# Kernel optimization log

Measured on AMD Instinct MI355X. Metric: run time of the kernel, lower is better.

Reference implementation:

```python
import jax, jax.numpy as jnp
import numpy as np

TEMPERATURE = 1.0


def setup_inputs() -> dict:
    key = jax.random.key(0)
    kq, kk, kv = jax.random.split(key, 3)
    shape = (2, 16, 2048, 64)  # B, H, L, D
    q = jax.random.normal(kq, shape, dtype=jnp.float32)
    k = jax.random.normal(kk, shape, dtype=jnp.float32)
    v = jax.random.normal(kv, shape, dtype=jnp.float32)
    return {"q": q, "k": k, "v": v}


def reference(q, k, v):
    # q, k, v: [B, H, L, D]
    L = q.shape[2]
    # scores: [B, H, L, L]; note: divided by temperature, NOT sqrt(D), per source
    scores = jnp.einsum("bhqd,bhkd->bhqk", q, k) / TEMPERATURE
    # causal mask: position j > i masked with -inf
    causal = jnp.tril(jnp.ones((L, L), dtype=bool))  # True = keep
    scores = jnp.where(causal, scores, -jnp.inf)
    attn = jax.nn.softmax(scores, axis=-1)
    out = jnp.einsum("bhqk,bhkd->bhqd", attn, v)
    return out
```

## Files before the change

kernel.cpp:

```cpp
#include <hip/hip_runtime.h>
#include <math.h>


typedef __attribute__((ext_vector_type(8))) _Float16 f16x8;
typedef __attribute__((ext_vector_type(4))) _Float16 f16x4;
typedef __attribute__((ext_vector_type(4))) float f32x4;
typedef __attribute__((ext_vector_type(16))) float f32x16;
typedef unsigned short u16;
typedef unsigned int u32;
typedef __attribute__((ext_vector_type(8))) u16 u16x8;
typedef __attribute__((ext_vector_type(4))) u32 u32x4;

constexpr int Lq = 2048;
constexpr int Dd = 64;
constexpr int KT = 64;
constexpr int BH = 32;
constexpr float LOG2E = 1.44269504088896f;

#define SWZB(row, bcol) ((((row) * 128) + (bcol)) ^ (((row) & 7) << 4))
#define SWZB64(row, bcol) ((((row) * 64) + (bcol)) ^ ((((row) >> 1) & 3) << 4))

#define GLOAD_LDS16(g, l)                                                     \
  __builtin_amdgcn_global_load_lds(                                           \
      (const __attribute__((address_space(1))) void*)(g),                     \
      (__attribute__((address_space(3))) void*)(l), 16, 0, 0)

static __device__ __forceinline__ u16 f2h(float x) {
  return __builtin_bit_cast(u16, (_Float16)x);
}

static __device__ __forceinline__ float tmax16(const f32x16& v) {
  float a = fmaxf(v[0], v[1]), b = fmaxf(v[2], v[3]);
  float c = fmaxf(v[4], v[5]), d = fmaxf(v[6], v[7]);
  float e = fmaxf(v[8], v[9]), f = fmaxf(v[10], v[11]);
  float g = fmaxf(v[12], v[13]), h = fmaxf(v[14], v[15]);
  a = fmaxf(a, b); c = fmaxf(c, d); e = fmaxf(e, f); g = fmaxf(g, h);
  return fmaxf(fmaxf(a, c), fmaxf(e, g));
}
static __device__ __forceinline__ float tsum16(const f32x16& v) {
  float a = v[0] + v[1], b = v[2] + v[3], c = v[4] + v[5], d = v[6] + v[7];
  float e = v[8] + v[9], f = v[10] + v[11], g = v[12] + v[13], h = v[14] + v[15];
  a += b; c += d; e += f; g += h;
  return (a + c) + (e + g);
}

constexpr int PREP_KB = (BH * Lq * Dd) / (256 * 16);

__global__ __launch_bounds__(256)
void attn_prep(const float* __restrict__ K, const float* __restrict__ V,
               u16* __restrict__ Kh, u16* __restrict__ VTh) {
  const int b = blockIdx.x;
  const int tid = threadIdx.x;
  if (b < PREP_KB) {
    const size_t base = ((size_t)b * 256 + tid) * 16;
    const f32x4* src = reinterpret_cast<const f32x4*>(K + base);
    u16x8 o0, o1;
    #pragma unroll
    for (int i = 0; i < 2; ++i) {
      const f32x4 a = src[i];
      #pragma unroll
      for (int j = 0; j < 4; ++j) o0[i * 4 + j] = f2h(a[j]);
    }
    #pragma unroll
    for (int i = 0; i < 2; ++i) {
      const f32x4 a = src[2 + i];
      #pragma unroll
      for (int j = 0; j < 4; ++j) o1[i * 4 + j] = f2h(a[j]);
    }
    *reinterpret_cast<u16x8*>(Kh + base) = o0;
    *reinterpret_cast<u16x8*>(Kh + base + 8) = o1;
  } else {
    __shared__ u16 lt[64][66];
    const int vb = b - PREP_KB;
    const int h = vb >> 5, tt = vb & 31;
    const float* Vt = V + ((size_t)h * Lq + tt * 64) * Dd;
    const int r = tid & 63, dg = tid >> 6;
    #pragma unroll
    for (int i = 0; i < 4; ++i) {
      const f32x4 a = *reinterpret_cast<const f32x4*>(Vt + (size_t)r * Dd + dg * 16 + i * 4);
      #pragma unroll
      for (int j = 0; j < 2; ++j) {
        const unsigned two =
            (unsigned)f2h(a[2 * j]) | ((unsigned)f2h(a[2 * j + 1]) << 16);
        *reinterpret_cast<unsigned*>(&lt[r][dg * 16 + i * 4 + j * 2]) = two;
      }
    }
    __syncthreads();
    const int d = tid >> 2, kq = tid & 3;
    u16x8 w0, w1;
    #pragma unroll
    for (int j = 0; j < 8; ++j) w0[j] = lt[kq * 16 + j][d];
    #pragma unroll
    for (int j = 0; j < 8; ++j) w1[j] = lt[kq * 16 + 8 + j][d];
    u16* dst = VTh + ((size_t)h * Dd + d) * Lq + tt * 64 + kq * 16;
    *reinterpret_cast<u16x8*>(dst) = w0;
    *reinterpret_cast<u16x8*>(dst + 8) = w1;
  }
}

__global__ __launch_bounds__(64)
void attn_main(const float* __restrict__ Q, float* __restrict__ O,
               const u16* __restrict__ Kh, const u16* __restrict__ VTh) {
  __shared__ char ksA[2][4096];
  __shared__ char vtA[2][4096];
  __shared__ float bc[32];

  const int lane = threadIdx.x;
  const int l31  = lane & 31;
  const int hi   = lane >> 5;

  const int b = blockIdx.x;
  const int chunk = 63 - (b >> 5);
  const int h = b & 31;

  const float* Qb = Q + (size_t)h * Lq * Dd;
  float*       Ob = O + (size_t)h * Lq * Dd;
  const u16*   Kb = Kh + (size_t)h * Lq * Dd;
  const u16*   Vb = VTh + (size_t)h * Dd * Lq;

  const int T    = chunk + 1;
  const int qrow = chunk * 32;

  f16x8 qf[4];
  #pragma unroll
  for (int kc = 0; kc < 4; ++kc) {
    const float* qp = Qb + (size_t)(qrow + l31) * Dd + kc * 16 + hi * 8;
    const f32x4 a = *reinterpret_cast<const f32x4*>(qp);
    const f32x4 c = *reinterpret_cast<const f32x4*>(qp + 4);
    f16x8 q8;
    #pragma unroll
    for (int e = 0; e < 4; ++e) {
      q8[e]     = (_Float16)(a[e] * LOG2E);
      q8[e + 4] = (_Float16)(c[e] * LOG2E);
    }
    qf[kc] = q8;
  }

  float m = -INFINITY, lsum = 0.f;
  f32x16 o0, o1;
  #pragma unroll
  for (int e = 0; e < 16; ++e) { o0[e] = 0.f; o1[e] = 0.f; }

  const int rrK = lane >> 3;
  const int c0K = (lane & 7) ^ (rrK & 7);
  const int rrV = lane >> 2;
  const int c0V = (lane & 3) ^ ((lane >> 3) & 3);

#define STAGE(t_, buf_)                                                       \
  do {                                                                        \
    const u16* Kt_ = Kb + (size_t)(t_) * 32 * Dd;                             \
    _Pragma("unroll")                                                         \
    for (int it = 0; it < 4; ++it) {                                          \
      GLOAD_LDS16(Kt_ + (size_t)(it * 8 + rrK) * Dd + c0K * 8,                \
                  &ksA[buf_][it * 1024 + lane * 16]);                         \
    }                                                                         \
    _Pragma("unroll")                                                         \
    for (int it = 0; it < 4; ++it) {                                          \
      GLOAD_LDS16(Vb + (size_t)(it * 16 + rrV) * Lq + (t_) * 32 + c0V * 8,    \
                  &vtA[buf_][it * 1024 + lane * 16]);                         \
    }                                                                         \
  } while (0)

  STAGE(0, 0);

  int cur = 0;
  #pragma unroll 1
  for (int t = 0; t < T; ++t) {
    const bool pf = (t + 1 < T);
    if (pf) {
      STAGE(t + 1, cur ^ 1);
      asm volatile("s_waitcnt vmcnt(8)" ::: "memory");
    } else {
      asm volatile("s_waitcnt vmcnt(0)" ::: "memory");
    }
    __builtin_amdgcn_sched_barrier(0);
    const char* kb = ksA[cur];
    const char* vb = vtA[cur];
    const bool last = (t == T - 1);

    f32x16 st0;
    #pragma unroll
    for (int e = 0; e < 16; ++e) st0[e] = 0.f;
    __builtin_amdgcn_s_setprio(1);
    #pragma unroll
    for (int kc = 0; kc < 4; ++kc) {
      const f16x8 kf = *reinterpret_cast<const f16x8*>(
          kb + SWZB(l31, kc * 32 + hi * 16));
      st0 = __builtin_amdgcn_mfma_f32_32x32x16_f16(kf, qf[kc], st0, 0, 0, 0);
    }
    __builtin_amdgcn_s_setprio(0);

    if (last) {
      #pragma unroll
      for (int r = 0; r < 16; ++r) {
        const int crow = (r & 3) + 8 * (r >> 2) + 4 * hi;
        if (crow > l31) st0[r] = -INFINITY;
      }
    }

    float pm = tmax16(st0);
    pm = fmaxf(pm, __shfl_xor(pm, 32));

    if (__any(pm > m + 8.f * LOG2E)) {
      const float mn = fmaxf(m, pm);
      const float sc = exp2f(m - mn);
      m = mn;
      lsum *= sc;
      if (hi == 0) bc[l31] = sc;
      const f32x4 s0 = *reinterpret_cast<const f32x4*>(&bc[4 * hi]);
      const f32x4 s1 = *reinterpret_cast<const f32x4*>(&bc[8 + 4 * hi]);
      const f32x4 s2 = *reinterpret_cast<const f32x4*>(&bc[16 + 4 * hi]);
      const f32x4 s3 = *reinterpret_cast<const f32x4*>(&bc[24 + 4 * hi]);
      #pragma unroll
      for (int r = 0; r < 16; ++r) {
        const float fac = (r < 4) ? s0[r & 3] : (r < 8) ? s1[r & 3]
                        : (r < 12) ? s2[r & 3] : s3[r & 3];
        o0[r] *= fac;
        o1[r] *= fac;
      }
    }

    #pragma unroll
    for (int r = 0; r < 16; ++r) st0[r] = exp2f(st0[r] - m);
    float rs = tsum16(st0);
    rs += __shfl_xor(rs, 32);
    lsum += rs;

    #pragma unroll
    for (int ks2 = 0; ks2 < 2; ++ks2) {
      const u32 pe0 = __builtin_bit_cast(u32,
          __builtin_amdgcn_cvt_pkrtz(st0[8 * ks2 + 0], st0[8 * ks2 + 1]));
      const u32 pe1 = __builtin_bit_cast(u32,
          __builtin_amdgcn_cvt_pkrtz(st0[8 * ks2 + 2], st0[8 * ks2 + 3]));
      const u32 po0 = __builtin_bit_cast(u32,
          __builtin_amdgcn_cvt_pkrtz(st0[8 * ks2 + 4], st0[8 * ks2 + 5]));
      const u32 po1 = __builtin_bit_cast(u32,
          __builtin_amdgcn_cvt_pkrtz(st0[8 * ks2 + 6], st0[8 * ks2 + 7]));
      const u32 ss0 = __shfl_xor(hi ? pe0 : po0, 32);
      const u32 ss1 = __shfl_xor(hi ? pe1 : po1, 32);
      u32x4 w;
      w[0] = hi ? ss0 : pe0;
      w[1] = hi ? ss1 : pe1;
      w[2] = hi ? po0 : ss0;
      w[3] = hi ? po1 : ss1;
      const f16x8 pa = __builtin_bit_cast(f16x8, w);
      const int cb = ks2 * 32 + hi * 16;
      const f16x8 v0 = *reinterpret_cast<const f16x8*>(vb + SWZB64(l31, cb));
      const f16x8 v1 = *reinterpret_cast<const f16x8*>(vb + SWZB64(32 + l31, cb));
      __builtin_amdgcn_s_setprio(1);
      o0 = __builtin_amdgcn_mfma_f32_32x32x16_f16(pa, v0, o0, 0, 0, 0);
      o1 = __builtin_amdgcn_mfma_f32_32x32x16_f16(pa, v1, o1, 0, 0, 0);
      __builtin_amdgcn_s_setprio(0);
    }
    cur ^= 1;
  }

  const float inv = 1.f / lsum;
  if (hi == 0) bc[l31] = inv;
  const f32x4 i0 = *reinterpret_cast<const f32x4*>(&bc[4 * hi]);
  const f32x4 i1 = *reinterpret_cast<const f32x4*>(&bc[8 + 4 * hi]);
  const f32x4 i2 = *reinterpret_cast<const f32x4*>(&bc[16 + 4 * hi]);
  const f32x4 i3 = *reinterpret_cast<const f32x4*>(&bc[24 + 4 * hi]);
  #pragma unroll
  for (int r = 0; r < 16; ++r) {
    const int crow = (r & 3) + 8 * (r >> 2) + 4 * hi;
    const float fac = (r < 4) ? i0[r & 3] : (r < 8) ? i1[r & 3]
                    : (r < 12) ? i2[r & 3] : i3[r & 3];
    float* op = Ob + (size_t)(qrow + crow) * Dd + l31;
    op[0]  = o0[r] * fac;
    op[32] = o1[r] * fac;
  }
#undef STAGE
}

__global__ __launch_bounds__(256)
void causal_attn_fb(const float* __restrict__ Q, const float* __restrict__ K,
                    const float* __restrict__ V, float* __restrict__ O) {
  __shared__ char ks[2][KT * 128];
  __shared__ char vt[2][Dd * 128];
  __shared__ char pl[4][16 * 128];
  const int tid = threadIdx.x, lane = tid & 63, wv = tid >> 6;
  const int l15 = lane & 15, g = lane >> 4;
  const int kg = tid & 15, dq = tid >> 4;
  const int bh = blockIdx.x / 16, pr = blockIdx.x % 16;
  const size_t base = (size_t)bh * Lq * Dd;
  const float* Qb = Q + base; const float* Kb = K + base;
  const float* Vb = V + base; float* Ob = O + base;
  char* pw = pl[wv];
  #pragma unroll 1
  for (int phase = 0; phase < 2; ++phase) {
    const int chunk = (phase == 0) ? pr : (31 - pr);
    const int row0 = chunk * 64, T = chunk + 1, qrow = row0 + wv * 16;
    f16x8 qf[2];
    #pragma unroll
    for (int kk = 0; kk < 2; ++kk) {
      const float* qp = Qb + (size_t)(qrow + l15) * Dd + kk * 32 + g * 8;
      const f32x4 a = *reinterpret_cast<const f32x4*>(qp);
      const f32x4 b = *reinterpret_cast<const f32x4*>(qp + 4);
      f16x8 q8;
      #pragma unroll
      for (int i = 0; i < 4; ++i) { q8[i] = (_Float16)a[i]; q8[i+4] = (_Float16)b[i]; }
      qf[kk] = q8;
    }
    float m[4], lsum[4]; f32x4 o[4];
    #pragma unroll
    for (int r = 0; r < 4; ++r) { m[r] = -INFINITY; lsum[r] = 0.f; }
    #pragma unroll
    for (int nd = 0; nd < 4; ++nd) o[nd] = f32x4{0.f, 0.f, 0.f, 0.f};
    {
      f32x4 kreg[4], vreg[4];
      #pragma unroll
      for (int i = 0; i < 4; ++i) {
        const int c = tid + i * 256;
        kreg[i] = *reinterpret_cast<const f32x4*>(Kb + (size_t)(c >> 4) * Dd + (c & 15) * 4);
      }
      #pragma unroll
      for (int c = 0; c < 4; ++c)
        vreg[c] = *reinterpret_cast<const f32x4*>(Vb + (size_t)(kg * 4 + c) * Dd + dq * 4);
      __syncthreads();
      #pragma unroll
      for (int i = 0; i < 4; ++i) {
        const int c = tid + i * 256;
        f16x4 hh;
        #pragma unroll
        for (int jj = 0; jj < 4; ++jj) hh[jj] = (_Float16)kreg[i][jj];
        *reinterpret_cast<f16x4*>(ks[0] + SWZB(c >> 4, (c & 15) * 8)) = hh;
      }
      #pragma unroll
      for (int jj = 0; jj < 4; ++jj) {
        f16x4 hh;
        #pragma unroll
        for (int c = 0; c < 4; ++c) hh[c] = (_Float16)vreg[c][jj];
        *reinterpret_cast<f16x4*>(vt[0] + SWZB(dq * 4 + jj, kg * 8)) = hh;
      }
    }
    int cur = 0;
    #pragma unroll 1
    for (int t = 0; t < T; ++t) {
      __syncthreads();
      const char* kb = ks[cur]; const char* vb = vt[cur];
      f32x4 kreg[4], vreg[4];
      const bool pfn = (t + 1 < T);
      if (pfn) {
        const float* Kt = Kb + (size_t)(t + 1) * KT * Dd;
        const float* Vt = Vb + (size_t)(t + 1) * KT * Dd;
        #pragma unroll
        for (int i = 0; i < 4; ++i) {
          const int c = tid + i * 256;
          kreg[i] = *reinterpret_cast<const f32x4*>(Kt + (size_t)(c >> 4) * Dd + (c & 15) * 4);
        }
        #pragma unroll
        for (int c = 0; c < 4; ++c)
          vreg[c] = *reinterpret_cast<const f32x4*>(Vt + (size_t)(kg * 4 + c) * Dd + dq * 4);
      }
      f32x4 s[4];
      #pragma unroll
      for (int n = 0; n < 4; ++n) s[n] = f32x4{0.f, 0.f, 0.f, 0.f};
      #pragma unroll
      for (int kk = 0; kk < 2; ++kk) {
        #pragma unroll
        for (int n = 0; n < 4; ++n) {
          const f16x8 kf = *reinterpret_cast<const f16x8*>(kb + SWZB(n * 16 + l15, kk * 64 + g * 16));
          s[n] = __builtin_amdgcn_mfma_f32_16x16x32_f16(qf[kk], kf, s[n], 0, 0, 0);
        }
      }
      if (t == T - 1) {
        #pragma unroll
        for (int n = 0; n < 4; ++n) {
          const int key = t * KT + n * 16 + l15;
          #pragma unroll
          for (int r = 0; r < 4; ++r)
            if (key > qrow + 4 * g + r) s[n][r] = -INFINITY;
        }
      }
      float rmax[4], rsum[4], scale[4];
      #pragma unroll
      for (int r = 0; r < 4; ++r)
        rmax[r] = fmaxf(fmaxf(s[0][r], s[1][r]), fmaxf(s[2][r], s[3][r]));
      #pragma unroll
      for (int mk = 1; mk <= 8; mk <<= 1) {
        #pragma unroll
        for (int r = 0; r < 4; ++r) rmax[r] = fmaxf(rmax[r], __shfl_xor(rmax[r], mk));
      }
      #pragma unroll
      for (int r = 0; r < 4; ++r) {
        const float mn = fmaxf(m[r], rmax[r]);
        scale[r] = __expf(m[r] - mn); m[r] = mn;
      }
      #pragma unroll
      for (int n = 0; n < 4; ++n) {
        #pragma unroll
        for (int r = 0; r < 4; ++r) s[n][r] = __expf(s[n][r] - m[r]);
      }
      #pragma unroll
      for (int r = 0; r < 4; ++r) rsum[r] = (s[0][r] + s[1][r]) + (s[2][r] + s[3][r]);
      #pragma unroll
      for (int mk = 1; mk <= 8; mk <<= 1) {
        #pragma unroll
        for (int r = 0; r < 4; ++r) rsum[r] += __shfl_xor(rsum[r], mk);
      }
      #pragma unroll
      for (int r = 0; r < 4; ++r) lsum[r] = lsum[r] * scale[r] + rsum[r];
      #pragma unroll
      for (int nd = 0; nd < 4; ++nd) {
        #pragma unroll
        for (int r = 0; r < 4; ++r) o[nd][r] *= scale[r];
      }
      #pragma unroll
      for (int n = 0; n < 4; ++n) {
        #pragma unroll
        for (int r = 0; r < 4; ++r)
          *reinterpret_cast<_Float16*>(pw + SWZB(4 * g + r, (n * 16 + l15) * 2)) = (_Float16)s[n][r];
      }
      asm volatile("s_waitcnt lgkmcnt(0)" ::: "memory");
      __builtin_amdgcn_sched_barrier(0);
      #pragma unroll
      for (int kblk = 0; kblk < 2; ++kblk) {
        const f16x8 pf = *reinterpret_cast<const f16x8*>(pw + SWZB(l15, kblk * 64 + g * 16));
        #pragma unroll
        for (int nd = 0; nd < 4; ++nd) {
          const f16x8 vf = *reinterpret_cast<const f16x8*>(vb + SWZB(nd * 16 + l15, kblk * 64 + g * 16));
          o[nd] = __builtin_amdgcn_mfma_f32_16x16x32_f16(pf, vf, o[nd], 0, 0, 0);
        }
      }
      if (pfn) {
        char* kn = ks[cur ^ 1]; char* vn = vt[cur ^ 1];
        #pragma unroll
        for (int i = 0; i < 4; ++i) {
          const int c = tid + i * 256;
          f16x4 hh;
          #pragma unroll
          for (int jj = 0; jj < 4; ++jj) hh[jj] = (_Float16)kreg[i][jj];
          *reinterpret_cast<f16x4*>(kn + SWZB(c >> 4, (c & 15) * 8)) = hh;
        }
        #pragma unroll
        for (int jj = 0; jj < 4; ++jj) {
          f16x4 hh;
          #pragma unroll
          for (int c = 0; c < 4; ++c) hh[c] = (_Float16)vreg[c][jj];
          *reinterpret_cast<f16x4*>(vn + SWZB(dq * 4 + jj, kg * 8)) = hh;
        }
      }
      cur ^= 1;
    }
    float inv[4];
    #pragma unroll
    for (int r = 0; r < 4; ++r) inv[r] = 1.f / lsum[r];
    #pragma unroll
    for (int nd = 0; nd < 4; ++nd) {
      #pragma unroll
      for (int r = 0; r < 4; ++r)
        Ob[(size_t)(qrow + 4 * g + r) * Dd + nd * 16 + l15] = o[nd][r] * inv[r];
    }
  }
}

extern "C" void kernel_launch(void* const* d_in, const int* in_sizes, int n_in,
                              void* d_out, int out_size, void* d_ws, size_t ws_size,
                              hipStream_t stream) {
  const float* q = (const float*)d_in[0];
  const float* k = (const float*)d_in[1];
  const float* v = (const float*)d_in[2];
  float* o = (float*)d_out;
  const size_t elems = (size_t)BH * Lq * Dd;
  const size_t need = elems * 2 * 2;
  if (ws_size >= need) {
    u16* Kh = (u16*)d_ws;
    u16* VTh = Kh + elems;
    attn_prep<<<dim3(2 * PREP_KB), dim3(256), 0, stream>>>(k, v, Kh, VTh);
    attn_main<<<dim3(BH * 64), dim3(64), 0, stream>>>(q, o, Kh, VTh);
  } else {
    causal_attn_fb<<<dim3(BH * 16), dim3(256), 0, stream>>>(q, k, v, o);
  }
  (void)in_sizes; (void)n_in; (void)out_size;
}
```

Measured before the change: 94.64 us.

## Load K/V fragments directly into registers and swizzle block-to-head mapping

```diff
diff --git a/kernel.cpp b/kernel.cpp
--- a/kernel.cpp
+++ b/kernel.cpp
@@ -18,12 +18,6 @@
 constexpr float LOG2E = 1.44269504088896f;
 
 #define SWZB(row, bcol) ((((row) * 128) + (bcol)) ^ (((row) & 7) << 4))
-#define SWZB64(row, bcol) ((((row) * 64) + (bcol)) ^ ((((row) >> 1) & 3) << 4))
-
-#define GLOAD_LDS16(g, l)                                                     \
-  __builtin_amdgcn_global_load_lds(                                           \
-      (const __attribute__((address_space(1))) void*)(g),                     \
-      (__attribute__((address_space(3))) void*)(l), 16, 0, 0)
 
 static __device__ __forceinline__ u16 f2h(float x) {
   return __builtin_bit_cast(u16, (_Float16)x);
@@ -101,17 +95,16 @@
 __global__ __launch_bounds__(64)
 void attn_main(const float* __restrict__ Q, float* __restrict__ O,
                const u16* __restrict__ Kh, const u16* __restrict__ VTh) {
-  __shared__ char ksA[2][4096];
-  __shared__ char vtA[2][4096];
   __shared__ float bc[32];
 
   const int lane = threadIdx.x;
   const int l31  = lane & 31;
   const int hi   = lane >> 5;
 
-  const int b = blockIdx.x;
-  const int chunk = 63 - (b >> 5);
-  const int h = b & 31;
+  const int bid = blockIdx.x;
+  const int swz = (bid & 7) * 256 + (bid >> 3);
+  const int h     = swz >> 6;
+  const int chunk = 63 - (swz & 63);
 
   const float* Qb = Q + (size_t)h * Lq * Dd;
   float*       Ob = O + (size_t)h * Lq * Dd;
@@ -141,118 +134,103 @@
   #pragma unroll
   for (int e = 0; e < 16; ++e) { o0[e] = 0.f; o1[e] = 0.f; }
 
-  const int rrK = lane >> 3;
-  const int c0K = (lane & 7) ^ (rrK & 7);
-  const int rrV = lane >> 2;
-  const int c0V = (lane & 3) ^ ((lane >> 3) & 3);
-
-#define STAGE(t_, buf_)                                                       \
+  const u16* Krow  = Kb + (size_t)l31 * Dd + hi * 8;
+  const u16* V0row = Vb + (size_t)l31 * Lq + hi * 8;
+  const u16* V1row = Vb + (size_t)(32 + l31) * Lq + hi * 8;
+
+#define LOADF(kf_, vf_, t_)                                                   \
   do {                                                                        \
-    const u16* Kt_ = Kb + (size_t)(t_) * 32 * Dd;                             \
+    const u16* kp_ = Krow + (size_t)(t_) * 32 * Dd;                           \
+    kf_[0] = *reinterpret_cast<const f16x8*>(kp_);                            \
+    kf_[1] = *reinterpret_cast<const f16x8*>(kp_ + 16);                       \
+    kf_[2] = *reinterpret_cast<const f16x8*>(kp_ + 32);                       \
+    kf_[3] = *reinterpret_cast<const f16x8*>(kp_ + 48);                       \
+    vf_[0] = *reinterpret_cast<const f16x8*>(V0row + (t_) * 32);              \
+    vf_[1] = *reinterpret_cast<const f16x8*>(V0row + (t_) * 32 + 16);         \
+    vf_[2] = *reinterpret_cast<const f16x8*>(V1row + (t_) * 32);              \
+    vf_[3] = *reinterpret_cast<const f16x8*>(V1row + (t_) * 32 + 16);         \
+  } while (0)
+
+#define COMPUTE_TILE(kf_, vf_, last_)                                         \
+  do {                                                                        \
+    f32x16 st0;                                                               \
     _Pragma("unroll")                                                         \
-    for (int it = 0; it < 4; ++it) {                                          \
-      GLOAD_LDS16(Kt_ + (size_t)(it * 8 + rrK) * Dd + c0K * 8,                \
-                  &ksA[buf_][it * 1024 + lane * 16]);                         \
+    for (int e = 0; e < 16; ++e) st0[e] = 0.f;                                \
+    __builtin_amdgcn_s_setprio(1);                                            \
+    _Pragma("unroll")                                                         \
+    for (int kc = 0; kc < 4; ++kc)                                            \
+      st0 = __builtin_amdgcn_mfma_f32_32x32x16_f16(kf_[kc], qf[kc], st0,      \
+                                                   0, 0, 0);                  \
+    __builtin_amdgcn_s_setprio(0);                                            \
+    if (last_) {                                                              \
+      _Pragma("unroll")                                                       \
+      for (int r = 0; r < 16; ++r) {                                          \
+        const int crow_ = (r & 3) + 8 * (r >> 2) + 4 * hi;                    \
+        if (crow_ > l31) st0[r] = -INFINITY;                                  \
+      }                                                                       \
+    }                                                                         \
+    float pm = tmax16(st0);                                                   \
+    pm = fmaxf(pm, __shfl_xor(pm, 32));                                       \
+    if (__any(pm > m + 8.f * LOG2E)) {                                        \
+      const float mn = fmaxf(m, pm);                                          \
+      const float sc = exp2f(m - mn);                                         \
+      m = mn;                                                                 \
+      lsum *= sc;                                                             \
+      if (hi == 0) bc[l31] = sc;                                              \
+      const f32x4 s0_ = *reinterpret_cast<const f32x4*>(&bc[4 * hi]);         \
+      const f32x4 s1_ = *reinterpret_cast<const f32x4*>(&bc[8 + 4 * hi]);     \
+      const f32x4 s2_ = *reinterpret_cast<const f32x4*>(&bc[16 + 4 * hi]);    \
+      const f32x4 s3_ = *reinterpret_cast<const f32x4*>(&bc[24 + 4 * hi]);    \
+      _Pragma("unroll")                                                       \
+      for (int r = 0; r < 16; ++r) {                                          \
+        const float fac = (r < 4) ? s0_[r & 3] : (r < 8) ? s1_[r & 3]         \
+                        : (r < 12) ? s2_[r & 3] : s3_[r & 3];                 \
+        o0[r] *= fac;                                                         \
+        o1[r] *= fac;                                                         \
+      }                                                                       \
     }                                                                         \
     _Pragma("unroll")                                                         \
-    for (int it = 0; it < 4; ++it) {                                          \
-      GLOAD_LDS16(Vb + (size_t)(it * 16 + rrV) * Lq + (t_) * 32 + c0V * 8,    \
-                  &vtA[buf_][it * 1024 + lane * 16]);                         \
+    for (int r = 0; r < 16; ++r) st0[r] = exp2f(st0[r] - m);                  \
+    float rs = tsum16(st0);                                                   \
+    rs += __shfl_xor(rs, 32);                                                 \
+    lsum += rs;                                                               \
+    _Pragma("unroll")                                                         \
+    for (int ks2 = 0; ks2 < 2; ++ks2) {                                       \
+      const u32 pe0 = __builtin_bit_cast(u32,                                 \
+          __builtin_amdgcn_cvt_pkrtz(st0[8 * ks2 + 0], st0[8 * ks2 + 1]));    \
+      const u32 pe1 = __builtin_bit_cast(u32,                                 \
+          __builtin_amdgcn_cvt_pkrtz(st0[8 * ks2 + 2], st0[8 * ks2 + 3]));    \
+      const u32 po0 = __builtin_bit_cast(u32,                                 \
+          __builtin_amdgcn_cvt_pkrtz(st0[8 * ks2 + 4], st0[8 * ks2 + 5]));    \
+      const u32 po1 = __builtin_bit_cast(u32,                                 \
+          __builtin_amdgcn_cvt_pkrtz(st0[8 * ks2 + 6], st0[8 * ks2 + 7]));    \
+      const u32 ss0 = __shfl_xor(hi ? pe0 : po0, 32);                         \
+      const u32 ss1 = __shfl_xor(hi ? pe1 : po1, 32);                         \
+      u32x4 w_;                                                               \
+      w_[0] = hi ? ss0 : pe0;                                                 \
+      w_[1] = hi ? ss1 : pe1;                                                 \
+      w_[2] = hi ? po0 : ss0;                                                 \
+      w_[3] = hi ? po1 : ss1;                                                 \
+      const f16x8 pa = __builtin_bit_cast(f16x8, w_);                         \
+      __builtin_amdgcn_s_setprio(1);                                          \
+      o0 = __builtin_amdgcn_mfma_f32_32x32x16_f16(pa, vf_[ks2], o0, 0, 0, 0); \
+      o1 = __builtin_amdgcn_mfma_f32_32x32x16_f16(pa, vf_[2 + ks2], o1,       \
+                                                  0, 0, 0);                   \
+      __builtin_amdgcn_s_setprio(0);                                          \
     }                                                                         \
   } while (0)
 
-  STAGE(0, 0);
-
-  int cur = 0;
+  f16x8 kA[4], vA[4], kB[4], vB[4];
+  LOADF(kA, vA, 0);
+  int t = 0;
   #pragma unroll 1
-  for (int t = 0; t < T; ++t) {
-    const bool pf = (t + 1 < T);
-    if (pf) {
-      STAGE(t + 1, cur ^ 1);
-      asm volatile("s_waitcnt vmcnt(8)" ::: "memory");
-    } else {
-      asm volatile("s_waitcnt vmcnt(0)" ::: "memory");
-    }
-    __builtin_amdgcn_sched_barrier(0);
-    const char* kb = ksA[cur];
-    const char* vb = vtA[cur];
-    const bool last = (t == T - 1);
-
-    f32x16 st0;
-    #pragma unroll
-    for (int e = 0; e < 16; ++e) st0[e] = 0.f;
-    __builtin_amdgcn_s_setprio(1);
-    #pragma unroll
-    for (int kc = 0; kc < 4; ++kc) {
-      const f16x8 kf = *reinterpret_cast<const f16x8*>(
-          kb + SWZB(l31, kc * 32 + hi * 16));
-      st0 = __builtin_amdgcn_mfma_f32_32x32x16_f16(kf, qf[kc], st0, 0, 0, 0);
-    }
-    __builtin_amdgcn_s_setprio(0);
-
-    if (last) {
-      #pragma unroll
-      for (int r = 0; r < 16; ++r) {
-        const int crow = (r & 3) + 8 * (r >> 2) + 4 * hi;
-        if (crow > l31) st0[r] = -INFINITY;
-      }
-    }
-
-    float pm = tmax16(st0);
-    pm = fmaxf(pm, __shfl_xor(pm, 32));
-
-    if (__any(pm > m + 8.f * LOG2E)) {
-      const float mn = fmaxf(m, pm);
-      const float sc = exp2f(m - mn);
-      m = mn;
-      lsum *= sc;
-      if (hi == 0) bc[l31] = sc;
-      const f32x4 s0 = *reinterpret_cast<const f32x4*>(&bc[4 * hi]);
-      const f32x4 s1 = *reinterpret_cast<const f32x4*>(&bc[8 + 4 * hi]);
-      const f32x4 s2 = *reinterpret_cast<const f32x4*>(&bc[16 + 4 * hi]);
-      const f32x4 s3 = *reinterpret_cast<const f32x4*>(&bc[24 + 4 * hi]);
-      #pragma unroll
-      for (int r = 0; r < 16; ++r) {
-        const float fac = (r < 4) ? s0[r & 3] : (r < 8) ? s1[r & 3]
-                        : (r < 12) ? s2[r & 3] : s3[r & 3];
-        o0[r] *= fac;
-        o1[r] *= fac;
-      }
-    }
-
-    #pragma unroll
-    for (int r = 0; r < 16; ++r) st0[r] = exp2f(st0[r] - m);
-    float rs = tsum16(st0);
-    rs += __shfl_xor(rs, 32);
-    lsum += rs;
-
-    #pragma unroll
-    for (int ks2 = 0; ks2 < 2; ++ks2) {
-      const u32 pe0 = __builtin_bit_cast(u32,
-          __builtin_amdgcn_cvt_pkrtz(st0[8 * ks2 + 0], st0[8 * ks2 + 1]));
-      const u32 pe1 = __builtin_bit_cast(u32,
-          __builtin_amdgcn_cvt_pkrtz(st0[8 * ks2 + 2], st0[8 * ks2 + 3]));
-      const u32 po0 = __builtin_bit_cast(u32,
-          __builtin_amdgcn_cvt_pkrtz(st0[8 * ks2 + 4], st0[8 * ks2 + 5]));
-      const u32 po1 = __builtin_bit_cast(u32,
-          __builtin_amdgcn_cvt_pkrtz(st0[8 * ks2 + 6], st0[8 * ks2 + 7]));
-      const u32 ss0 = __shfl_xor(hi ? pe0 : po0, 32);
-      const u32 ss1 = __shfl_xor(hi ? pe1 : po1, 32);
-      u32x4 w;
-      w[0] = hi ? ss0 : pe0;
-      w[1] = hi ? ss1 : pe1;
-      w[2] = hi ? po0 : ss0;
-      w[3] = hi ? po1 : ss1;
-      const f16x8 pa = __builtin_bit_cast(f16x8, w);
-      const int cb = ks2 * 32 + hi * 16;
-      const f16x8 v0 = *reinterpret_cast<const f16x8*>(vb + SWZB64(l31, cb));
-      const f16x8 v1 = *reinterpret_cast<const f16x8*>(vb + SWZB64(32 + l31, cb));
-      __builtin_amdgcn_s_setprio(1);
-      o0 = __builtin_amdgcn_mfma_f32_32x32x16_f16(pa, v0, o0, 0, 0, 0);
-      o1 = __builtin_amdgcn_mfma_f32_32x32x16_f16(pa, v1, o1, 0, 0, 0);
-      __builtin_amdgcn_s_setprio(0);
-    }
-    cur ^= 1;
+  while (true) {
+    if (t + 1 < T) LOADF(kB, vB, t + 1);
+    COMPUTE_TILE(kA, vA, t == T - 1);
+    if (++t == T) break;
+    if (t + 1 < T) LOADF(kA, vA, t + 1);
+    COMPUTE_TILE(kB, vB, t == T - 1);
+    if (++t == T) break;
   }
 
   const float inv = 1.f / lsum;
@@ -270,7 +248,8 @@
     op[0]  = o0[r] * fac;
     op[32] = o1[r] * fac;
   }
-#undef STAGE
+#undef LOADF
+#undef COMPUTE_TILE
 }
 
 __global__ __launch_bounds__(256)
```

Result: slower. 113.3 us (+19.7%).
